# Performance work log

Hardware: AMD Instinct MI355X
Metric: run time of the kernel (lower is better)

The kernel has to match this reference:

```python
import jax, jax.numpy as jnp
import numpy as np

NUM_T = 1000   # num_timesteps == timesteps -> skip = 1, seq = range(0, 1000)
ETA = 0.1
BETA_START, BETA_END = 1e-4, 0.02


def _ddim_schedule():
    # get_beta_schedule: linspace in float64, then cast
    betas = np.linspace(BETA_START, BETA_END, NUM_T, dtype=np.float64)
    # compute_alpha prepends beta=0 -> alpha_cumprod[0] = 1.0, indexed at t+1
    alph = np.concatenate([[1.0], np.cumprod(1.0 - betas)]).astype(np.float32)
    seq = np.arange(NUM_T)
    seq_next = np.concatenate([[-1], seq[:-1]])
    at = alph[seq + 1]
    at_next = alph[seq_next + 1]   # t=-1 -> alph[0] = 1.0
    # loop iterates reversed(seq) x reversed(seq_next)
    return (jnp.asarray(at[::-1].copy()),
            jnp.asarray(at_next[::-1].copy()),
            jnp.asarray(seq[::-1].copy(), dtype=jnp.int32))


def setup_inputs() -> dict:
    key = jax.random.key(0)
    k1, k2, k3, k4, k5 = jax.random.split(key, 5)
    n, c, s, h, w = 2, 3, 8, 64, 44
    return {
        "skes": jax.random.normal(k1, (n, c, s, h, w), dtype=jnp.float32),
        "sil_T": jax.random.normal(k2, (n * s, 1, h, w), dtype=jnp.float32),
        "w_skes": jax.random.normal(k3, (c,), dtype=jnp.float32),
        "w_sil": jax.random.normal(k4, (), dtype=jnp.float32),
        "t_scale": jax.random.normal(k5, (), dtype=jnp.float32),
    }


def reference(skes, sil_T, w_skes, w_sil, t_scale):
    n, c, s, h, w = skes.shape
    # rearrange 'n c s h w -> (n s) c h w'
    skes2 = jnp.transpose(skes, (0, 2, 1, 3, 4)).reshape(n * s, c, h, w)
    # surrogate denoiser condition: 1x1 channel projection of the skeleton maps
    cond = jnp.einsum('nchw,c->nhw', skes2, w_skes)[:, None]  # (n*s,1,h,w)
    at_r, atn_r, idx_r = _ddim_schedule()
    noise_key = jax.random.key(42)

    def model(sil_t, t_val):
        t_emb = t_scale * (t_val.astype(jnp.float32) / NUM_T)
        return jnp.tanh(cond + w_sil * sil_t + t_emb)

    def step(sil_t, x):
        at, atn, idx = x
        sil_0 = model(sil_t, idx)
        # NOTE: original uses the FIXED initial noise sil_T here (not sil_t)
        et = (sil_T - jnp.sqrt(at) * sil_0) / jnp.sqrt(1.0 - at)
        c1 = ETA * jnp.sqrt((1.0 - at / atn) * (1.0 - atn) / (1.0 - at))
        c2 = jnp.sqrt(jnp.maximum(1.0 - atn - c1 * c1, 0.0))
        noise = jax.random.normal(jax.random.fold_in(noise_key, idx),
                                  sil_T.shape, dtype=sil_T.dtype)
        sil_next = jnp.sqrt(atn) * sil_0 + c1 * noise + c2 * et
        return sil_next, sil_0

    _, preds = jax.lax.scan(step, sil_T, (at_r, atn_r, idx_r))
    # preds: (1000, n*s, 1, h, w) == stacked list of per-step sil_0 predictions
    return preds
```

## Files before the change

### kernel.cpp

```cpp
#include <hip/hip_runtime.h>
#include <cstdint>

#define NSTEP 1000
#define NELEM 45056
#define HW    2816
#define EPB   64
#define PW    4
#define BLK   ((PW + 1) * 64)
#define WIN   40
#define NWIN  (NSTEP / WIN)

struct AlphTab { float a[NSTEP + 1]; };

constexpr AlphTab make_alph() {
    AlphTab t{};
    t.a[0] = 1.0f;
    double alph = 1.0;
    const double start = 1e-4, stop = 0.02;
    const double step = (stop - start) / 999.0;
    for (int i = 0; i < NSTEP; ++i) {
        double beta = (i == NSTEP - 1) ? stop : ((double)i * step + start);
        alph *= (1.0 - beta);
        t.a[i + 1] = (float)alph;
    }
    return t;
}
constexpr AlphTab ALPH = make_alph();

__device__ __forceinline__ void tf20(uint32_t K0, uint32_t K1, uint32_t K2,
                                     uint32_t& x0, uint32_t& x1) {
    x0 += K0; x1 += K1;
#define TFR(r) { x0 += x1; x1 = ((x1 << r) | (x1 >> (32 - r))); x1 ^= x0; }
    TFR(13) TFR(15) TFR(26) TFR(6)
    x0 += K1; x1 += K2 + 1u;
    TFR(17) TFR(29) TFR(16) TFR(24)
    x0 += K2; x1 += K0 + 2u;
    TFR(13) TFR(15) TFR(26) TFR(6)
    x0 += K0; x1 += K1 + 3u;
    TFR(17) TFR(29) TFR(16) TFR(24)
    x0 += K1; x1 += K2 + 4u;
    TFR(13) TFR(15) TFR(26) TFR(6)
    x0 += K2; x1 += K0 + 5u;
#undef TFR
}

__device__ __forceinline__ float bits_to_erfinv(uint32_t bits) {
    const float f2 = __uint_as_float((bits >> 9) | 0x3F800000u) - 1.0f;
    const float u  = f2 * 2.0f - 0.99999994f;
    const float t1 = (1.0f - u) * (1.0f + u);
    const float w  = __log2f(t1) * -0.6931472f;
    const bool  lt = w < 5.0f;
    const float sw = __builtin_amdgcn_sqrtf(w);
    const float ww = lt ? (w - 2.5f) : (sw - 3.0f);
    float p =          lt ?  2.81022636e-08f : -0.000200214257f;
    p = fmaf(p, ww,    lt ?  3.43273939e-07f :  0.000100950558f);
    p = fmaf(p, ww,    lt ? -3.5233877e-06f  :  0.00134934322f);
    p = fmaf(p, ww,    lt ? -4.39150654e-06f : -0.00367342844f);
    p = fmaf(p, ww,    lt ?  0.00021858087f  :  0.00573950773f);
    p = fmaf(p, ww,    lt ? -0.00125372503f  : -0.0076224613f);
    p = fmaf(p, ww,    lt ? -0.00417768164f  :  0.00943887047f);
    p = fmaf(p, ww,    lt ?  0.246640727f    :  1.00167406f);
    p = fmaf(p, ww,    lt ?  1.50140941f     :  2.83297682f);
    return p * u;
}

__global__ __launch_bounds__(BLK)
void fused_kernel(const float* __restrict__ skes,
                  const float* __restrict__ silT,
                  const float* __restrict__ wskes,
                  const float* __restrict__ wsil_p,
                  const float* __restrict__ tsc_p,
                  float* __restrict__ out) {
    __shared__ __align__(16) uint32_t tab[NSTEP][8];
    __shared__ __align__(16) float dbuf[2][WIN][EPB];

    const float wsil = wsil_p[0];
    const float tsc  = tsc_p[0];
    const float L2E2 = 2.8853900817779268f;

    for (int k = (int)threadIdx.x; k < NSTEP; k += BLK) {
        const int t = 999 - k;
        const float at  = ALPH.a[t + 1];
        const float atn = ALPH.a[t];
        const float c1 = 0.1f * sqrtf((1.0f - at / atn) * (1.0f - atn) / (1.0f - at));
        const float c2 = sqrtf(fmaxf(1.0f - atn - c1 * c1, 0.0f));
        const float rs = 1.0f / sqrtf(1.0f - at);
        const float A  = sqrtf(atn) - c2 * sqrtf(at) * rs;
        const float e  = c2 * rs;
        const float temb = tsc * ((float)t / 1000.0f);
        uint32_t k0 = 0u, k1 = (uint32_t)t;
        tf20(0u, 42u, 0x1BD11BDAu ^ 42u, k0, k1);
        tab[k][0] = __float_as_uint(c1 * 1.4142135f);
        tab[k][1] = __float_as_uint(e);
        tab[k][2] = k0;
        tab[k][3] = k1;
        tab[k][4] = __float_as_uint(A);
        tab[k][5] = __float_as_uint(temb * L2E2);
        tab[k][6] = k0 ^ k1 ^ 0x1BD11BDAu;
        tab[k][7] = 0u;
    }

    const int wid  = (int)(threadIdx.x >> 6);
    const int lane = (int)(threadIdx.x & 63);
    const int j    = (int)(blockIdx.x * EPB) + lane;

    const float sT = silT[j];

    float cc2 = 0.0f, ws2 = 0.0f, sil = 0.0f;
    if (wid == PW) {
        const int ns = j / HW;
        const int hw = j - ns * HW;
        const int n  = ns >> 3;
        const int ss = ns & 7;
        const float* sk = skes + (size_t)((n * 3) * 8 + ss) * HW + hw;
        const float w0 = wskes[0], w1 = wskes[1], w2 = wskes[2];
        const float cond = fmaf(w2, sk[2 * 8 * HW], fmaf(w1, sk[8 * HW], w0 * sk[0]));
        cc2 = cond * L2E2;
        ws2 = wsil * L2E2;
        sil = sT;
    }

    __syncthreads();

    if (wid < PW) {
        float* db = &dbuf[0][0][0];
#pragma unroll 2
        for (int kk = wid; kk < WIN; kk += PW) {
            const uint4 ta    = *(const uint4*)&tab[kk][0];
            const uint32_t k2 = tab[kk][6];
            uint32_t x0 = 0u, x1 = (uint32_t)j;
            tf20(ta.z, ta.w, k2, x0, x1);
            const float ei = bits_to_erfinv(x0 ^ x1);
            db[kk * EPB + lane] =
                fmaf(__uint_as_float(ta.x), ei, __uint_as_float(ta.y) * sT);
        }
    }
    __syncthreads();

    float* op = out + j;

    for (int w = 0; w < NWIN; ++w) {
        if (wid < PW) {
            if (w + 1 < NWIN) {
                float* db = &dbuf[(w + 1) & 1][0][0];
                const int kbase = (w + 1) * WIN;
#pragma unroll 2
                for (int kk = wid; kk < WIN; kk += PW) {
                    const int k = kbase + kk;
                    const uint4 ta    = *(const uint4*)&tab[k][0];
                    const uint32_t k2 = tab[k][6];
                    uint32_t x0 = 0u, x1 = (uint32_t)j;
                    tf20(ta.z, ta.w, k2, x0, x1);
                    const float ei = bits_to_erfinv(x0 ^ x1);
                    db[kk * EPB + lane] =
                        fmaf(__uint_as_float(ta.x), ei, __uint_as_float(ta.y) * sT);
                }
            }
        } else {
            const float* db = &dbuf[w & 1][0][0];
            const int kbase = w * WIN;
#pragma unroll 4
            for (int kk = 0; kk < WIN; ++kk) {
                const uint2 tt = *(const uint2*)&tab[kbase + kk][4];
                const float A  = __uint_as_float(tt.x);
                const float tb = __uint_as_float(tt.y);
                const float e2 = __builtin_amdgcn_exp2f(fmaf(ws2, sil, cc2 + tb));
                const float r  = __builtin_amdgcn_rcpf(e2 + 1.0f);
                const float s0 = fmaf(-2.0f, r, 1.0f);
                *op = s0; op += NELEM;
                sil = fmaf(A, s0, db[kk * EPB + lane]);
            }
        }
        __syncthreads();
    }
}

extern "C" void kernel_launch(void* const* d_in, const int* in_sizes, int n_in,
                              void* d_out, int out_size, void* d_ws, size_t ws_size,
                              hipStream_t stream) {
    const float* skes = (const float*)d_in[0];
    const float* silT = (const float*)d_in[1];
    const float* wsk  = (const float*)d_in[2];
    const float* wsil = (const float*)d_in[3];
    const float* tsc  = (const float*)d_in[4];
    float* out = (float*)d_out;
    (void)in_sizes; (void)n_in; (void)out_size; (void)d_ws; (void)ws_size;

    dim3 grid(NELEM / EPB), block(BLK);
    hipLaunchKernelGGL(fused_kernel, grid, block, 0, stream,
                       skes, silT, wsk, wsil, tsc, out);
}
```

Measured before the change: 334.9 us.

## Double producer waves, split table into SoA arrays, branch erfinv tail

```diff
diff --git a/kernel.cpp b/kernel.cpp
--- a/kernel.cpp
+++ b/kernel.cpp
@@ -5,9 +5,10 @@
 #define NELEM 45056
 #define HW    2816
 #define EPB   64
-#define PW    4
+#define PW    8
 #define BLK   ((PW + 1) * 64)
 #define WIN   40
+#define SPP   (WIN / PW)
 #define NWIN  (NSTEP / WIN)
 
 struct AlphTab { float a[NSTEP + 1]; };
@@ -50,17 +51,33 @@
     const float t1 = (1.0f - u) * (1.0f + u);
     const float w  = __log2f(t1) * -0.6931472f;
     const bool  lt = w < 5.0f;
-    const float sw = __builtin_amdgcn_sqrtf(w);
-    const float ww = lt ? (w - 2.5f) : (sw - 3.0f);
-    float p =          lt ?  2.81022636e-08f : -0.000200214257f;
-    p = fmaf(p, ww,    lt ?  3.43273939e-07f :  0.000100950558f);
-    p = fmaf(p, ww,    lt ? -3.5233877e-06f  :  0.00134934322f);
-    p = fmaf(p, ww,    lt ? -4.39150654e-06f : -0.00367342844f);
-    p = fmaf(p, ww,    lt ?  0.00021858087f  :  0.00573950773f);
-    p = fmaf(p, ww,    lt ? -0.00125372503f  : -0.0076224613f);
-    p = fmaf(p, ww,    lt ? -0.00417768164f  :  0.00943887047f);
-    p = fmaf(p, ww,    lt ?  0.246640727f    :  1.00167406f);
-    p = fmaf(p, ww,    lt ?  1.50140941f     :  2.83297682f);
+
+    const float wwn = w - 2.5f;
+    float pn =           2.81022636e-08f;
+    pn = fmaf(pn, wwn,   3.43273939e-07f);
+    pn = fmaf(pn, wwn,  -3.5233877e-06f);
+    pn = fmaf(pn, wwn,  -4.39150654e-06f);
+    pn = fmaf(pn, wwn,   0.00021858087f);
+    pn = fmaf(pn, wwn,  -0.00125372503f);
+    pn = fmaf(pn, wwn,  -0.00417768164f);
+    pn = fmaf(pn, wwn,   0.246640727f);
+    pn = fmaf(pn, wwn,   1.50140941f);
+
+    float p = pn;
+    if (__any(!lt)) {
+        const float sw  = __builtin_amdgcn_sqrtf(w);
+        const float wwf = sw - 3.0f;
+        float pf =           -0.000200214257f;
+        pf = fmaf(pf, wwf,    0.000100950558f);
+        pf = fmaf(pf, wwf,    0.00134934322f);
+        pf = fmaf(pf, wwf,   -0.00367342844f);
+        pf = fmaf(pf, wwf,    0.00573950773f);
+        pf = fmaf(pf, wwf,   -0.0076224613f);
+        pf = fmaf(pf, wwf,    0.00943887047f);
+        pf = fmaf(pf, wwf,    1.00167406f);
+        pf = fmaf(pf, wwf,    2.83297682f);
+        p = lt ? pn : pf;
+    }
     return p * u;
 }
 
@@ -71,8 +88,10 @@
                   const float* __restrict__ wsil_p,
                   const float* __restrict__ tsc_p,
                   float* __restrict__ out) {
-    __shared__ __align__(16) uint32_t tab[NSTEP][8];
-    __shared__ __align__(16) float dbuf[2][WIN][EPB];
+    __shared__ __align__(16) uint4    tabP[NSTEP];
+    __shared__            uint32_t    tabK2[NSTEP];
+    __shared__ __align__(8)  uint2    tabC[NSTEP];
+    __shared__ __align__(16) float    dbuf[2][WIN][EPB];
 
     const float wsil = wsil_p[0];
     const float tsc  = tsc_p[0];
@@ -90,14 +109,10 @@
         const float temb = tsc * ((float)t / 1000.0f);
         uint32_t k0 = 0u, k1 = (uint32_t)t;
         tf20(0u, 42u, 0x1BD11BDAu ^ 42u, k0, k1);
-        tab[k][0] = __float_as_uint(c1 * 1.4142135f);
-        tab[k][1] = __float_as_uint(e);
-        tab[k][2] = k0;
-        tab[k][3] = k1;
-        tab[k][4] = __float_as_uint(A);
-        tab[k][5] = __float_as_uint(temb * L2E2);
-        tab[k][6] = k0 ^ k1 ^ 0x1BD11BDAu;
-        tab[k][7] = 0u;
+        tabP[k]  = make_uint4(__float_as_uint(c1 * 1.4142135f),
+                              __float_as_uint(e), k0, k1);
+        tabK2[k] = k0 ^ k1 ^ 0x1BD11BDAu;
+        tabC[k]  = make_uint2(__float_as_uint(A), __float_as_uint(temb * L2E2));
     }
 
     const int wid  = (int)(threadIdx.x >> 6);
@@ -124,10 +139,11 @@
 
     if (wid < PW) {
         float* db = &dbuf[0][0][0];
-#pragma unroll 2
-        for (int kk = wid; kk < WIN; kk += PW) {
-            const uint4 ta    = *(const uint4*)&tab[kk][0];
-            const uint32_t k2 = tab[kk][6];
+#pragma unroll
+        for (int s = 0; s < SPP; ++s) {
+            const int kk = wid + s * PW;
+            const uint4 ta    = tabP[kk];
+            const uint32_t k2 = tabK2[kk];
             uint32_t x0 = 0u, x1 = (uint32_t)j;
             tf20(ta.z, ta.w, k2, x0, x1);
             const float ei = bits_to_erfinv(x0 ^ x1);
@@ -144,11 +160,12 @@
             if (w + 1 < NWIN) {
                 float* db = &dbuf[(w + 1) & 1][0][0];
                 const int kbase = (w + 1) * WIN;
-#pragma unroll 2
-                for (int kk = wid; kk < WIN; kk += PW) {
-                    const int k = kbase + kk;
-                    const uint4 ta    = *(const uint4*)&tab[k][0];
-                    const uint32_t k2 = tab[k][6];
+#pragma unroll
+                for (int s = 0; s < SPP; ++s) {
+                    const int kk = wid + s * PW;
+                    const int k  = kbase + kk;
+                    const uint4 ta    = tabP[k];
+                    const uint32_t k2 = tabK2[k];
                     uint32_t x0 = 0u, x1 = (uint32_t)j;
                     tf20(ta.z, ta.w, k2, x0, x1);
                     const float ei = bits_to_erfinv(x0 ^ x1);
@@ -161,7 +178,7 @@
             const int kbase = w * WIN;
 #pragma unroll 4
             for (int kk = 0; kk < WIN; ++kk) {
-                const uint2 tt = *(const uint2*)&tab[kbase + kk][4];
+                const uint2 tt = tabC[kbase + kk];
                 const float A  = __uint_as_float(tt.x);
                 const float tb = __uint_as_float(tt.y);
                 const float e2 = __builtin_amdgcn_exp2f(fmaf(ws2, sil, cc2 + tb));
```

Measured after the change: 321.4 us. -4.0%, faster.
